# Performance work log

Measured on AMD Instinct MI355X. Metric: run time of the kernel, lower is better.

The kernel has to match this reference:

```python
import jax, jax.numpy as jnp
import numpy as np

DIM = 256
NHEAD = 8
HDIM = DIM // NHEAD
WS = 8
EPS = 1e-6
LN_EPS = 1e-5


def _layer_norm(x, g, b):
    m = x.mean(-1, keepdims=True)
    v = ((x - m) ** 2).mean(-1, keepdims=True)
    return (x - m) / jnp.sqrt(v + LN_EPS) * g + b


def _encoder_layer(x, Wq, Wk, Wv, Wm, Wmlp1, Wmlp2, g1, b1, g2, b2):
    # x: [n, L, C] windows; LoFTR encoder layer with linear (elu+1) attention
    n, L, C = x.shape
    q = (x @ Wq).reshape(n, L, NHEAD, HDIM)
    k = (x @ Wk).reshape(n, L, NHEAD, HDIM)
    v = (x @ Wv).reshape(n, L, NHEAD, HDIM)
    Q = jax.nn.elu(q) + 1.0
    K = jax.nn.elu(k) + 1.0
    v = v / L
    KV = jnp.einsum('nshd,nshv->nhdv', K, v)           # [n,H,D,D]
    Z = 1.0 / (jnp.einsum('nlhd,nhd->nlh', Q, K.sum(axis=1)) + EPS)
    msg = jnp.einsum('nlhd,nhdv,nlh->nlhv', Q, KV, Z) * L  # [n,L,H,D]
    msg = msg.reshape(n, L, C) @ Wm
    msg = _layer_norm(msg, g1, b1)
    h = jnp.concatenate([x, msg], axis=-1) @ Wmlp1     # [n,L,2C]
    h = jax.nn.relu(h) @ Wmlp2                          # [n,L,C]
    msg = _layer_norm(h, g2, b2)
    return msg + x


def setup_inputs() -> dict:
    key = jax.random.key(0)
    ks = jax.random.split(key, 12)
    B, Hh, Ww, C = 4, 240, 240, DIM
    x = jax.random.normal(ks[0], (B, Hh * Ww, C), dtype=jnp.float32)
    s = 0.02
    return {
        'x': x,
        'Wq': jax.random.normal(ks[1], (C, C), dtype=jnp.float32) * s,
        'Wk': jax.random.normal(ks[2], (C, C), dtype=jnp.float32) * s,
        'Wv': jax.random.normal(ks[3], (C, C), dtype=jnp.float32) * s,
        'Wm': jax.random.normal(ks[4], (C, C), dtype=jnp.float32) * s,
        'Wmlp1': jax.random.normal(ks[5], (2 * C, 2 * C), dtype=jnp.float32) * s,
        'Wmlp2': jax.random.normal(ks[6], (2 * C, C), dtype=jnp.float32) * s,
        'g1': jnp.ones((C,), dtype=jnp.float32),
        'b1': jnp.zeros((C,), dtype=jnp.float32),
        'g2': jnp.ones((C,), dtype=jnp.float32),
        'b2': jnp.zeros((C,), dtype=jnp.float32),
        'H': 240,
        'W': 240,
        'y': 0,
    }


def reference(x, Wq, Wk, Wv, Wm, Wmlp1, Wmlp2, g1, b1, g2, b2, H, W, y):
    B, N, C = x.shape
    # H, W chosen divisible by WS -> pad_r = pad_b = 0 (no-pad branch)
    _h, _w = H // WS, W // WS
    xw = x.reshape(B, _h, WS, _w, WS, C)
    xw = xw.transpose(0, 1, 3, 2, 4, 5).reshape(B * _h * _w, WS * WS, C)
    out = _encoder_layer(xw, Wq, Wk, Wv, Wm, Wmlp1, Wmlp2, g1, b1, g2, b2)
    out = out.reshape(B, _h, _w, WS, WS, C)
    out = out.transpose(0, 1, 3, 2, 4, 5).reshape(B, N, C)
    return out
```

## Files before the change

kernel.cpp:

```cpp
#include <hip/hip_runtime.h>

typedef unsigned short u16;
typedef unsigned int   u32;
typedef __attribute__((ext_vector_type(8))) short bf16x8;
typedef __attribute__((ext_vector_type(4))) float f32x4;

#define ATT_EPS 1e-6f
#define LN_EPS  1e-5f
#define MFMA16  __builtin_amdgcn_mfma_f32_16x16x32_bf16

__device__ __forceinline__ float bflo(u32 u){ return __uint_as_float(u << 16); }
__device__ __forceinline__ float bfhi(u32 u){ return __uint_as_float(u & 0xffff0000u); }
__device__ __forceinline__ u16 f2b(float f){
  u32 x = __float_as_uint(f);
  return (u16)((x + 0x7fffu + ((x >> 16) & 1u)) >> 16);
}
__device__ __forceinline__ float elup1(float x){ return x > 0.f ? x + 1.f : __expf(x); }
__device__ __forceinline__ bf16x8 as_bf(uint4 u){ union { uint4 a; bf16x8 b; } c; c.a = u; return c.b; }
__device__ __forceinline__ uint2 pack4(float a, float b, float c, float d){
  return make_uint2((u32)f2b(a) | ((u32)f2b(b) << 16),
                    (u32)f2b(c) | ((u32)f2b(d) << 16));
}

__device__ __forceinline__ int AO(int l, int cb){ return l*512 + (cb ^ ((l & 7) << 4)); }
__device__ __forceinline__ int TO(int c, int sb){ return c*128 + (sb ^ ((c & 7) << 4)); }
__device__ __forceinline__ int KVO(int h, int v, int db){ return h*4096 + v*64 + (db ^ ((v & 3) << 4)); }

__device__ __forceinline__ void qtr(float v[4], int qi){
  float x0 = __shfl_xor(v[0],1), x1 = __shfl_xor(v[1],1),
        x2 = __shfl_xor(v[2],1), x3 = __shfl_xor(v[3],1);
  if (qi & 1){ v[0]=x1; v[2]=x3; } else { v[1]=x0; v[3]=x2; }
  float y0 = __shfl_xor(v[0],2), y1 = __shfl_xor(v[1],2),
        y2 = __shfl_xor(v[2],2), y3 = __shfl_xor(v[3],2);
  if (qi & 2){ v[0]=y2; v[1]=y3; } else { v[2]=y0; v[3]=y1; }
}

__global__ __launch_bounds__(256)
void packw(const float* __restrict__ Wk, const float* __restrict__ Wv,
           const float* __restrict__ Wq, const float* __restrict__ Wm,
           const float* __restrict__ W1, const float* __restrict__ W2,
           uint4* __restrict__ ws)
{
  const int g = blockIdx.x*256 + threadIdx.x;
  const int tile = g >> 6, lane = g & 63;
  const float* src; int Nd, base, tl;
  if      (tile <  128){ src=Wk; Nd=256; base=0;     tl=tile;      }
  else if (tile <  256){ src=Wv; Nd=256; base=8192;  tl=tile-128;  }
  else if (tile <  384){ src=Wq; Nd=256; base=16384; tl=tile-256;  }
  else if (tile <  512){ src=Wm; Nd=256; base=24576; tl=tile-384;  }
  else if (tile < 1024){ src=W1; Nd=512; base=32768; tl=tile-512;  }
  else                 { src=W2; Nd=256; base=65536; tl=tile-1024; }
  const int KS = (tile >= 512) ? 16 : 8;
  const int nt = tl / KS, ks = tl - nt*KS;
  const int k0 = ks*32 + (lane >> 4)*8;
  const int n  = nt*16 + (lane & 15);
  u32 w[4];
  #pragma unroll
  for (int p = 0; p < 4; ++p){
    const u32 lo = f2b(src[(k0 + 2*p    )*Nd + n]);
    const u32 hi = f2b(src[(k0 + 2*p + 1)*Nd + n]);
    w[p] = lo | (hi << 16);
  }
  ws[base + (nt*KS + ks)*64 + lane] = make_uint4(w[0], w[1], w[2], w[3]);
}

__global__ __launch_bounds__(256, 2)
void lgattn_mfma(const float* __restrict__ xg, const uint4* __restrict__ wpk,
                 const float* __restrict__ g1v, const float* __restrict__ b1v,
                 const float* __restrict__ g2v, const float* __restrict__ b2v,
                 float* __restrict__ outg)
{
  __shared__ __align__(16) char  lds0[32768];
  __shared__ __align__(16) char  lds1[32768];
  __shared__ __align__(16) float ksum[256];
  __shared__ __align__(16) float denb[512];
  __shared__ __align__(16) float ps[256];

  const int t    = threadIdx.x;
  const int lane = t & 63;
  const int wid  = t >> 6;
  const int wm   = wid >> 1, wn = wid & 1;
  const int l15  = lane & 15, g4 = lane >> 4;
  const int qi   = lane & 3,  qq = (lane >> 2) & 3;
  const int rowA = 32*wm;
  const int wbn  = 8*wn;

  const int win = blockIdx.x;
  const int b   = win / 900;
  const int rem = win - b*900;
  const int wh  = rem / 30;
  const int ww  = rem - wh*30;
  const long long rowbase = ((long long)b*240 + wh*8)*240 + ww*8;

  const f32x4 fz = {0.f, 0.f, 0.f, 0.f};

  {
    const int r0 = wid*16, c0 = lane*4;
    #pragma unroll
    for (int i = 0; i < 16; ++i){
      const int l = r0 + i;
      const long long row = rowbase + (l >> 3)*240 + (l & 7);
      const float4 u = *(const float4*)(xg + row*256 + c0);
      *(uint2*)(lds0 + AO(l, c0*2)) = pack4(u.x, u.y, u.z, u.w);
    }
  }
  __syncthreads();

  bf16x8 xf[2][8];
  #pragma unroll
  for (int mt = 0; mt < 2; ++mt)
    #pragma unroll
    for (int ks = 0; ks < 8; ++ks)
      xf[mt][ks] = as_bf(*(const uint4*)(lds0 + AO(rowA + mt*16 + l15, ks*64 + g4*16)));
  __syncthreads();

  {
    f32x4 acc[8][2];
    #pragma unroll
    for (int nt = 0; nt < 8; ++nt){ acc[nt][0] = fz; acc[nt][1] = fz; }
    #pragma unroll
    for (int ks = 0; ks < 8; ++ks)
      #pragma unroll
      for (int nt = 0; nt < 8; ++nt){
        const bf16x8 bv = as_bf(wpk[((wbn + nt)*8 + ks)*64 + lane]);
        acc[nt][0] = MFMA16(xf[0][ks], bv, acc[nt][0], 0, 0, 0);
        acc[nt][1] = MFMA16(xf[1][ks], bv, acc[nt][1], 0, 0, 0);
      }
    #pragma unroll
    for (int nt = 0; nt < 8; ++nt)
      #pragma unroll
      for (int mt = 0; mt < 2; ++mt){
        const int c  = 128*wn + nt*16 + l15;
        const int sb = (rowA + mt*16 + 4*g4)*2;
        *(uint2*)(lds1 + TO(c, sb)) =
          pack4(elup1(acc[nt][mt][0]), elup1(acc[nt][mt][1]),
                elup1(acc[nt][mt][2]), elup1(acc[nt][mt][3]));
      }
  }
  {
    f32x4 acc[8][2];
    #pragma unroll
    for (int nt = 0; nt < 8; ++nt){ acc[nt][0] = fz; acc[nt][1] = fz; }
    #pragma unroll
    for (int ks = 0; ks < 8; ++ks)
      #pragma unroll
      for (int nt = 0; nt < 8; ++nt){
        const bf16x8 bv = as_bf(wpk[8192 + ((wbn + nt)*8 + ks)*64 + lane]);
        acc[nt][0] = MFMA16(xf[0][ks], bv, acc[nt][0], 0, 0, 0);
        acc[nt][1] = MFMA16(xf[1][ks], bv, acc[nt][1], 0, 0, 0);
      }
    #pragma unroll
    for (int nt = 0; nt < 8; ++nt)
      #pragma unroll
      for (int mt = 0; mt < 2; ++mt){
        const int c  = 128*wn + nt*16 + l15;
        const int sb = (rowA + mt*16 + 4*g4)*2;
        *(uint2*)(lds0 + TO(c, sb)) =
          pack4(acc[nt][mt][0], acc[nt][mt][1], acc[nt][mt][2], acc[nt][mt][3]);
      }
  }
  __syncthreads();

  {
    float s = 0.f;
    #pragma unroll
    for (int j = 0; j < 8; ++j){
      const uint4 u = *(const uint4*)(lds1 + TO(t, j*16));
      s += bflo(u.x)+bfhi(u.x)+bflo(u.y)+bfhi(u.y)
         + bflo(u.z)+bfhi(u.z)+bflo(u.w)+bfhi(u.w);
    }
    ksum[t] = s;
  }
  __syncthreads();

  {
    #pragma unroll
    for (int hh = 0; hh < 2; ++hh){
      const int h = 2*wid + hh;
      f32x4 acc[2][2];
      acc[0][0]=fz; acc[0][1]=fz; acc[1][0]=fz; acc[1][1]=fz;
      #pragma unroll
      for (int ks = 0; ks < 2; ++ks){
        bf16x8 a[2], bb[2];
        #pragma unroll
        for (int mt = 0; mt < 2; ++mt)
          a[mt]  = as_bf(*(const uint4*)(lds1 + TO(h*32 + mt*16 + l15, ks*64 + g4*16)));
        #pragma unroll
        for (int nt = 0; nt < 2; ++nt)
          bb[nt] = as_bf(*(const uint4*)(lds0 + TO(h*32 + nt*16 + l15, ks*64 + g4*16)));
        #pragma unroll
        for (int mt = 0; mt < 2; ++mt)
          #pragma unroll
          for (int nt = 0; nt < 2; ++nt)
            acc[mt][nt] = MFMA16(a[mt], bb[nt], acc[mt][nt], 0, 0, 0);
      }
      #pragma unroll
      for (int mt = 0; mt < 2; ++mt)
        #pragma unroll
        for (int nt = 0; nt < 2; ++nt){
          const int v  = nt*16 + l15;
          const int db = (mt*16 + 4*g4)*2;
          *(uint2*)(lds1 + KVO(h, v, db)) =
            pack4(acc[mt][nt][0], acc[mt][nt][1], acc[mt][nt][2], acc[mt][nt][3]);
        }
    }
  }
  __syncthreads();

  {
    f32x4 acc[8][2];
    #pragma unroll
    for (int nt = 0; nt < 8; ++nt){ acc[nt][0] = fz; acc[nt][1] = fz; }
    #pragma unroll
    for (int ks = 0; ks < 8; ++ks)
      #pragma unroll
      for (int nt = 0; nt < 8; ++nt){
        const bf16x8 bv = as_bf(wpk[16384 + ((wbn + nt)*8 + ks)*64 + lane]);
        acc[nt][0] = MFMA16(xf[0][ks], bv, acc[nt][0], 0, 0, 0);
        acc[nt][1] = MFMA16(xf[1][ks], bv, acc[nt][1], 0, 0, 0);
      }
    #pragma unroll
    for (int nt = 0; nt < 8; ++nt)
      #pragma unroll
      for (int mt = 0; mt < 2; ++mt){
        float v[4];
        #pragma unroll
        for (int r = 0; r < 4; ++r) v[r] = elup1(acc[nt][mt][r]);
        qtr(v, qi);
        const int l  = rowA + mt*16 + 4*g4 + qi;
        const int cb = (128*wn + nt*16 + 4*qq)*2;
        *(uint2*)(lds0 + AO(l, cb)) = pack4(v[0], v[1], v[2], v[3]);
      }
  }

  {
    const int dl = rowA + (lane & 31);
    #pragma unroll
    for (int hh = 0; hh < 2; ++hh){
      const int h = 4*wn + 2*(lane >> 5) + hh;
      float s = ATT_EPS;
      #pragma unroll
      for (int j = 0; j < 4; ++j){
        const uint4  qv = *(const uint4*)(lds0 + AO(dl, h*64 + j*16));
        const float4 k0 = *(const float4*)&ksum[h*32 + j*8];
        const float4 k1 = *(const float4*)&ksum[h*32 + j*8 + 4];
        s += bflo(qv.x)*k0.x + bfhi(qv.x)*k0.y + bflo(qv.y)*k0.z + bfhi(qv.y)*k0.w
           + bflo(qv.z)*k1.x + bfhi(qv.z)*k1.y + bflo(qv.w)*k1.z + bfhi(qv.w)*k1.w;
      }
      denb[dl*8 + h] = s;
    }
  }

  {
    f32x4 nacc[4][2][2];
    #pragma unroll
    for (int hh = 0; hh < 4; ++hh)
      #pragma unroll
      for (int mt = 0; mt < 2; ++mt)
        #pragma unroll
        for (int nt = 0; nt < 2; ++nt) nacc[hh][mt][nt] = fz;
    #pragma unroll
    for (int hh = 0; hh < 4; ++hh){
      const int h = 4*wn + hh;
      bf16x8 a[2], bb[2];
      #pragma unroll
      for (int mt = 0; mt < 2; ++mt)
        a[mt]  = as_bf(*(const uint4*)(lds0 + AO(rowA + mt*16 + l15, h*64 + g4*16)));
      #pragma unroll
      for (int nt = 0; nt < 2; ++nt)
        bb[nt] = as_bf(*(const uint4*)(lds1 + KVO(h, nt*16 + l15, g4*16)));
      #pragma unroll
      for (int mt = 0; mt < 2; ++mt)
        #pragma unroll
        for (int nt = 0; nt < 2; ++nt)
          nacc[hh][mt][nt] = MFMA16(a[mt], bb[nt], nacc[hh][mt][nt], 0, 0, 0);
    }
    __syncthreads();
    #pragma unroll
    for (int hh = 0; hh < 4; ++hh){
      const int h = 4*wn + hh;
      #pragma unroll
      for (int mt = 0; mt < 2; ++mt){
        const int   l  = rowA + mt*16 + 4*g4 + qi;
        const float rd = 1.0f / denb[l*8 + h];
        #pragma unroll
        for (int nt = 0; nt < 2; ++nt){
          float v[4];
          #pragma unroll
          for (int r = 0; r < 4; ++r) v[r] = nacc[hh][mt][nt][r];
          qtr(v, qi);
          const int cb = (h*32 + nt*16 + 4*qq)*2;
          *(uint2*)(lds1 + AO(l, cb)) = pack4(v[0]*rd, v[1]*rd, v[2]*rd, v[3]*rd);
        }
      }
    }
  }
  __syncthreads();

  {
    f32x4 macc[8][2];
    #pragma unroll
    for (int nt = 0; nt < 8; ++nt){ macc[nt][0] = fz; macc[nt][1] = fz; }
    #pragma unroll 2
    for (int ks = 0; ks < 8; ++ks){
      const bf16x8 a0 = as_bf(*(const uint4*)(lds1 + AO(rowA      + l15, ks*64 + g4*16)));
      const bf16x8 a1 = as_bf(*(const uint4*)(lds1 + AO(rowA + 16 + l15, ks*64 + g4*16)));
      #pragma unroll
      for (int nt = 0; nt < 8; ++nt){
        const bf16x8 bv = as_bf(wpk[24576 + ((wbn + nt)*8 + ks)*64 + lane]);
        macc[nt][0] = MFMA16(a0, bv, macc[nt][0], 0, 0, 0);
        macc[nt][1] = MFMA16(a1, bv, macc[nt][1], 0, 0, 0);
      }
    }
    float sm[2][4], sv[2][4];
    #pragma unroll
    for (int mt = 0; mt < 2; ++mt)
      #pragma unroll
      for (int r = 0; r < 4; ++r){
        float s = 0.f, q = 0.f;
        #pragma unroll
        for (int nt = 0; nt < 8; ++nt){ const float x = macc[nt][mt][r]; s += x; q += x*x; }
        #pragma unroll
        for (int m = 1; m < 16; m <<= 1){ s += __shfl_xor(s, m); q += __shfl_xor(q, m); }
        sm[mt][r] = s; sv[mt][r] = q;
      }
    if (l15 == 0){
      #pragma unroll
      for (int mt = 0; mt < 2; ++mt)
        #pragma unroll
        for (int r = 0; r < 4; ++r){
          const int row = rowA + mt*16 + 4*g4 + r;
          *(float2*)&ps[(row*2 + wn)*2] = make_float2(sm[mt][r], sv[mt][r]);
        }
    }
    __syncthreads();
    float mean[2][4], rstd[2][4];
    #pragma unroll
    for (int mt = 0; mt < 2; ++mt)
      #pragma unroll
      for (int r = 0; r < 4; ++r){
        const int row = rowA + mt*16 + 4*g4 + r;
        const float2 p0 = *(const float2*)&ps[(row*2 + 0)*2];
        const float2 p1 = *(const float2*)&ps[(row*2 + 1)*2];
        const float st = p0.x + p1.x, qt = p0.y + p1.y;
        const float mn = st * (1.f/256.f);
        mean[mt][r] = mn;
        rstd[mt][r] = rsqrtf(qt*(1.f/256.f) - mn*mn + LN_EPS);
      }
    #pragma unroll
    for (int mt = 0; mt < 2; ++mt){
      const int l = rowA + mt*16 + 4*g4 + qi;
      #pragma unroll
      for (int nt = 0; nt < 8; ++nt){
        float v[4];
        #pragma unroll
        for (int r = 0; r < 4; ++r) v[r] = (macc[nt][mt][r] - mean[mt][r]) * rstd[mt][r];
        qtr(v, qi);
        const int c = 128*wn + nt*16 + 4*qq;
        const float4 gg = *(const float4*)(g1v + c);
        const float4 bb = *(const float4*)(b1v + c);
        *(uint2*)(lds1 + AO(l, c*2)) =
          pack4(v[0]*gg.x + bb.x, v[1]*gg.y + bb.y, v[2]*gg.z + bb.z, v[3]*gg.w + bb.w);
      }
    }
  }
  __syncthreads();

  f32x4 oacc[8][2];
  #pragma unroll
  for (int nt = 0; nt < 8; ++nt){ oacc[nt][0] = fz; oacc[nt][1] = fz; }

  #pragma unroll
  for (int jt = 0; jt < 2; ++jt){
    f32x4 hacc[8][2];
    #pragma unroll
    for (int nt = 0; nt < 8; ++nt){ hacc[nt][0] = fz; hacc[nt][1] = fz; }
    const int w1base = 32768 + (jt*16 + wbn)*16*64;
    #pragma unroll
    for (int ks = 0; ks < 8; ++ks)
      #pragma unroll
      for (int nt = 0; nt < 8; ++nt){
        const bf16x8 bv = as_bf(wpk[w1base + (nt*16 + ks)*64 + lane]);
        hacc[nt][0] = MFMA16(xf[0][ks], bv, hacc[nt][0], 0, 0, 0);
        hacc[nt][1] = MFMA16(xf[1][ks], bv, hacc[nt][1], 0, 0, 0);
      }
    #pragma unroll 2
    for (int ks = 0; ks < 8; ++ks){
      const bf16x8 a0 = as_bf(*(const uint4*)(lds1 + AO(rowA      + l15, ks*64 + g4*16)));
      const bf16x8 a1 = as_bf(*(const uint4*)(lds1 + AO(rowA + 16 + l15, ks*64 + g4*16)));
      #pragma unroll
      for (int nt = 0; nt < 8; ++nt){
        const bf16x8 bv = as_bf(wpk[w1base + (nt*16 + 8 + ks)*64 + lane]);
        hacc[nt][0] = MFMA16(a0, bv, hacc[nt][0], 0, 0, 0);
        hacc[nt][1] = MFMA16(a1, bv, hacc[nt][1], 0, 0, 0);
      }
    }
    #pragma unroll
    for (int mt = 0; mt < 2; ++mt){
      const int l = rowA + mt*16 + 4*g4 + qi;
      #pragma unroll
      for (int nt = 0; nt < 8; ++nt){
        float v[4];
        #pragma unroll
        for (int r = 0; r < 4; ++r) v[r] = fmaxf(hacc[nt][mt][r], 0.f);
        qtr(v, qi);
        const int cb = (128*wn + nt*16 + 4*qq)*2;
        *(uint2*)(lds0 + AO(l, cb)) = pack4(v[0], v[1], v[2], v[3]);
      }
    }
    __syncthreads();
    #pragma unroll 2
    for (int ks = 0; ks < 8; ++ks){
      const bf16x8 a0 = as_bf(*(const uint4*)(lds0 + AO(rowA      + l15, ks*64 + g4*16)));
      const bf16x8 a1 = as_bf(*(const uint4*)(lds0 + AO(rowA + 16 + l15, ks*64 + g4*16)));
      #pragma unroll
      for (int nt = 0; nt < 8; ++nt){
        const bf16x8 bv = as_bf(wpk[65536 + ((wbn + nt)*16 + jt*8 + ks)*64 + lane]);
        oacc[nt][0] = MFMA16(a0, bv, oacc[nt][0], 0, 0, 0);
        oacc[nt][1] = MFMA16(a1, bv, oacc[nt][1], 0, 0, 0);
      }
    }
    if (jt == 0) __syncthreads();
  }

  {
    float sm[2][4], sv[2][4];
    #pragma unroll
    for (int mt = 0; mt < 2; ++mt)
      #pragma unroll
      for (int r = 0; r < 4; ++r){
        float s = 0.f, q = 0.f;
        #pragma unroll
        for (int nt = 0; nt < 8; ++nt){ const float x = oacc[nt][mt][r]; s += x; q += x*x; }
        #pragma unroll
        for (int m = 1; m < 16; m <<= 1){ s += __shfl_xor(s, m); q += __shfl_xor(q, m); }
        sm[mt][r] = s; sv[mt][r] = q;
      }
    __syncthreads();
    if (l15 == 0){
      #pragma unroll
      for (int mt = 0; mt < 2; ++mt)
        #pragma unroll
        for (int r = 0; r < 4; ++r){
          const int row = rowA + mt*16 + 4*g4 + r;
          *(float2*)&ps[(row*2 + wn)*2] = make_float2(sm[mt][r], sv[mt][r]);
        }
    }
    __syncthreads();
    float mean[2][4], rstd[2][4];
    #pragma unroll
    for (int mt = 0; mt < 2; ++mt)
      #pragma unroll
      for (int r = 0; r < 4; ++r){
        const int row = rowA + mt*16 + 4*g4 + r;
        const float2 p0 = *(const float2*)&ps[(row*2 + 0)*2];
        const float2 p1 = *(const float2*)&ps[(row*2 + 1)*2];
        const float st = p0.x + p1.x, qt = p0.y + p1.y;
        const float mn = st * (1.f/256.f);
        mean[mt][r] = mn;
        rstd[mt][r] = rsqrtf(qt*(1.f/256.f) - mn*mn + LN_EPS);
      }
    #pragma unroll
    for (int mt = 0; mt < 2; ++mt){
      const int l = rowA + mt*16 + 4*g4 + qi;
      const long long row = rowbase + (l >> 3)*240 + (l & 7);
      #pragma unroll
      for (int nt = 0; nt < 8; ++nt){
        float v[4];
        #pragma unroll
        for (int r = 0; r < 4; ++r) v[r] = (oacc[nt][mt][r] - mean[mt][r]) * rstd[mt][r];
        qtr(v, qi);
        const int c = 128*wn + nt*16 + 4*qq;
        const float4 gg = *(const float4*)(g2v + c);
        const float4 bb = *(const float4*)(b2v + c);
        const float4 xu = *(const float4*)(xg + row*256 + c);
        float4 st;
        st.x = v[0]*gg.x + bb.x + xu.x;
        st.y = v[1]*gg.y + bb.y + xu.y;
        st.z = v[2]*gg.z + bb.z + xu.z;
        st.w = v[3]*gg.w + bb.w + xu.w;
        *(float4*)(outg + row*256 + c) = st;
      }
    }
  }
}

extern "C" void kernel_launch(void* const* d_in, const int* in_sizes, int n_in,
                              void* d_out, int out_size, void* d_ws, size_t ws_size,
                              hipStream_t stream) {
  const float* xg = (const float*)d_in[0];
  const float* Wq = (const float*)d_in[1];
  const float* Wk = (const float*)d_in[2];
  const float* Wv = (const float*)d_in[3];
  const float* Wm = (const float*)d_in[4];
  const float* W1 = (const float*)d_in[5];
  const float* W2 = (const float*)d_in[6];
  const float* g1 = (const float*)d_in[7];
  const float* b1 = (const float*)d_in[8];
  const float* g2 = (const float*)d_in[9];
  const float* b2 = (const float*)d_in[10];

  uint4* wpk = (uint4*)d_ws;
  packw<<<dim3(320), dim3(256), 0, stream>>>(Wk, Wv, Wq, Wm, W1, W2, wpk);

  const int B = in_sizes[0] / (240 * 240 * 256);
  lgattn_mfma<<<dim3(B * 900), dim3(256), 0, stream>>>(xg, wpk, g1, b1, g2, b2, (float*)d_out);
}
```

Before: 1.488 ms.

## Use 8 waves per window block and fuse K-sum into KV computation

Doubles the block to 512 threads (8 waves in a 2x4 grid), so each wave computes half as many output column tiles in every GEMM stage, and the layer-norm partial sums are reduced across 4 column waves. The K column sum is now computed inside the per-head KV MFMA pass from the same loaded fragments, which removes one barrier and a separate LDS pass. The intent is more waves in flight to hide latency and fewer accumulator registers per wave, at the cost of more weight-fragment reloads per block and a tighter register budget under launch_bounds(512,4). Some loops are also fully unrolled.

```diff
diff --git a/kernel.cpp b/kernel.cpp
--- a/kernel.cpp
+++ b/kernel.cpp
@@ -64,7 +64,7 @@
   ws[base + (nt*KS + ks)*64 + lane] = make_uint4(w[0], w[1], w[2], w[3]);
 }
 
-__global__ __launch_bounds__(256, 2)
+__global__ __launch_bounds__(512, 4)
 void lgattn_mfma(const float* __restrict__ xg, const uint4* __restrict__ wpk,
                  const float* __restrict__ g1v, const float* __restrict__ b1v,
                  const float* __restrict__ g2v, const float* __restrict__ b2v,
@@ -74,16 +74,16 @@
   __shared__ __align__(16) char  lds1[32768];
   __shared__ __align__(16) float ksum[256];
   __shared__ __align__(16) float denb[512];
-  __shared__ __align__(16) float ps[256];
+  __shared__ __align__(16) float ps[512];
 
   const int t    = threadIdx.x;
   const int lane = t & 63;
   const int wid  = t >> 6;
-  const int wm   = wid >> 1, wn = wid & 1;
+  const int wm   = wid >> 2, wn = wid & 3;
   const int l15  = lane & 15, g4 = lane >> 4;
   const int qi   = lane & 3,  qq = (lane >> 2) & 3;
   const int rowA = 32*wm;
-  const int wbn  = 8*wn;
+  const int wbn  = 4*wn;
 
   const int win = blockIdx.x;
   const int b   = win / 900;
@@ -95,9 +95,9 @@
   const f32x4 fz = {0.f, 0.f, 0.f, 0.f};
 
   {
-    const int r0 = wid*16, c0 = lane*4;
-    #pragma unroll
-    for (int i = 0; i < 16; ++i){
+    const int r0 = wid*8, c0 = lane*4;
+    #pragma unroll
+    for (int i = 0; i < 8; ++i){
       const int l = r0 + i;
       const long long row = rowbase + (l >> 3)*240 + (l & 7);
       const float4 u = *(const float4*)(xg + row*256 + c0);
@@ -115,22 +115,22 @@
   __syncthreads();
 
   {
-    f32x4 acc[8][2];
-    #pragma unroll
-    for (int nt = 0; nt < 8; ++nt){ acc[nt][0] = fz; acc[nt][1] = fz; }
+    f32x4 acc[4][2];
+    #pragma unroll
+    for (int nt = 0; nt < 4; ++nt){ acc[nt][0] = fz; acc[nt][1] = fz; }
     #pragma unroll
     for (int ks = 0; ks < 8; ++ks)
       #pragma unroll
-      for (int nt = 0; nt < 8; ++nt){
+      for (int nt = 0; nt < 4; ++nt){
         const bf16x8 bv = as_bf(wpk[((wbn + nt)*8 + ks)*64 + lane]);
         acc[nt][0] = MFMA16(xf[0][ks], bv, acc[nt][0], 0, 0, 0);
         acc[nt][1] = MFMA16(xf[1][ks], bv, acc[nt][1], 0, 0, 0);
       }
     #pragma unroll
-    for (int nt = 0; nt < 8; ++nt)
+    for (int nt = 0; nt < 4; ++nt)
       #pragma unroll
       for (int mt = 0; mt < 2; ++mt){
-        const int c  = 128*wn + nt*16 + l15;
+        const int c  = 64*wn + nt*16 + l15;
         const int sb = (rowA + mt*16 + 4*g4)*2;
         *(uint2*)(lds1 + TO(c, sb)) =
           pack4(elup1(acc[nt][mt][0]), elup1(acc[nt][mt][1]),
@@ -138,22 +138,22 @@
       }
   }
   {
-    f32x4 acc[8][2];
-    #pragma unroll
-    for (int nt = 0; nt < 8; ++nt){ acc[nt][0] = fz; acc[nt][1] = fz; }
+    f32x4 acc[4][2];
+    #pragma unroll
+    for (int nt = 0; nt < 4; ++nt){ acc[nt][0] = fz; acc[nt][1] = fz; }
     #pragma unroll
     for (int ks = 0; ks < 8; ++ks)
       #pragma unroll
-      for (int nt = 0; nt < 8; ++nt){
+      for (int nt = 0; nt < 4; ++nt){
         const bf16x8 bv = as_bf(wpk[8192 + ((wbn + nt)*8 + ks)*64 + lane]);
         acc[nt][0] = MFMA16(xf[0][ks], bv, acc[nt][0], 0, 0, 0);
         acc[nt][1] = MFMA16(xf[1][ks], bv, acc[nt][1], 0, 0, 0);
       }
     #pragma unroll
-    for (int nt = 0; nt < 8; ++nt)
+    for (int nt = 0; nt < 4; ++nt)
       #pragma unroll
       for (int mt = 0; mt < 2; ++mt){
-        const int c  = 128*wn + nt*16 + l15;
+        const int c  = 64*wn + nt*16 + l15;
         const int sb = (rowA + mt*16 + 4*g4)*2;
         *(uint2*)(lds0 + TO(c, sb)) =
           pack4(acc[nt][mt][0], acc[nt][mt][1], acc[nt][mt][2], acc[nt][mt][3]);
@@ -162,65 +162,65 @@
   __syncthreads();
 
   {
-    float s = 0.f;
-    #pragma unroll
-    for (int j = 0; j < 8; ++j){
-      const uint4 u = *(const uint4*)(lds1 + TO(t, j*16));
-      s += bflo(u.x)+bfhi(u.x)+bflo(u.y)+bfhi(u.y)
-         + bflo(u.z)+bfhi(u.z)+bflo(u.w)+bfhi(u.w);
-    }
-    ksum[t] = s;
+    const int h = wid;
+    f32x4 acc[2][2];
+    acc[0][0]=fz; acc[0][1]=fz; acc[1][0]=fz; acc[1][1]=fz;
+    uint4 araw[2][2];
+    #pragma unroll
+    for (int ks = 0; ks < 2; ++ks)
+      #pragma unroll
+      for (int mt = 0; mt < 2; ++mt)
+        araw[ks][mt] = *(const uint4*)(lds1 + TO(h*32 + mt*16 + l15, ks*64 + g4*16));
+    #pragma unroll
+    for (int ks = 0; ks < 2; ++ks){
+      bf16x8 bb[2];
+      #pragma unroll
+      for (int nt = 0; nt < 2; ++nt)
+        bb[nt] = as_bf(*(const uint4*)(lds0 + TO(h*32 + nt*16 + l15, ks*64 + g4*16)));
+      #pragma unroll
+      for (int mt = 0; mt < 2; ++mt)
+        #pragma unroll
+        for (int nt = 0; nt < 2; ++nt)
+          acc[mt][nt] = MFMA16(as_bf(araw[ks][mt]), bb[nt], acc[mt][nt], 0, 0, 0);
+    }
+    float sm0 = 0.f, sm1 = 0.f;
+    #pragma unroll
+    for (int ks = 0; ks < 2; ++ks){
+      const uint4 u0 = araw[ks][0], u1 = araw[ks][1];
+      sm0 += bflo(u0.x)+bfhi(u0.x)+bflo(u0.y)+bfhi(u0.y)
+           + bflo(u0.z)+bfhi(u0.z)+bflo(u0.w)+bfhi(u0.w);
+      sm1 += bflo(u1.x)+bfhi(u1.x)+bflo(u1.y)+bfhi(u1.y)
+           + bflo(u1.z)+bfhi(u1.z)+bflo(u1.w)+bfhi(u1.w);
+    }
+    sm0 += __shfl_xor(sm0, 16); sm0 += __shfl_xor(sm0, 32);
+    sm1 += __shfl_xor(sm1, 16); sm1 += __shfl_xor(sm1, 32);
+    if (lane < 16){ ksum[h*32 + l15] = sm0; ksum[h*32 + 16 + l15] = sm1; }
+    #pragma unroll
+    for (int mt = 0; mt < 2; ++mt)
+      #pragma unroll
+      for (int nt = 0; nt < 2; ++nt){
+        const int v  = nt*16 + l15;
+        const int db = (mt*16 + 4*g4)*2;
+        *(uint2*)(lds1 + KVO(h, v, db)) =
+          pack4(acc[mt][nt][0], acc[mt][nt][1], acc[mt][nt][2], acc[mt][nt][3]);
+      }
   }
   __syncthreads();
 
   {
-    #pragma unroll
-    for (int hh = 0; hh < 2; ++hh){
-      const int h = 2*wid + hh;
-      f32x4 acc[2][2];
-      acc[0][0]=fz; acc[0][1]=fz; acc[1][0]=fz; acc[1][1]=fz;
-      #pragma unroll
-      for (int ks = 0; ks < 2; ++ks){
-        bf16x8 a[2], bb[2];
-        #pragma unroll
-        for (int mt = 0; mt < 2; ++mt)
-          a[mt]  = as_bf(*(const uint4*)(lds1 + TO(h*32 + mt*16 + l15, ks*64 + g4*16)));
-        #pragma unroll
-        for (int nt = 0; nt < 2; ++nt)
-          bb[nt] = as_bf(*(const uint4*)(lds0 + TO(h*32 + nt*16 + l15, ks*64 + g4*16)));
-        #pragma unroll
-        for (int mt = 0; mt < 2; ++mt)
-          #pragma unroll
-          for (int nt = 0; nt < 2; ++nt)
-            acc[mt][nt] = MFMA16(a[mt], bb[nt], acc[mt][nt], 0, 0, 0);
-      }
-      #pragma unroll
-      for (int mt = 0; mt < 2; ++mt)
-        #pragma unroll
-        for (int nt = 0; nt < 2; ++nt){
-          const int v  = nt*16 + l15;
-          const int db = (mt*16 + 4*g4)*2;
-          *(uint2*)(lds1 + KVO(h, v, db)) =
-            pack4(acc[mt][nt][0], acc[mt][nt][1], acc[mt][nt][2], acc[mt][nt][3]);
-        }
-    }
-  }
-  __syncthreads();
-
-  {
-    f32x4 acc[8][2];
-    #pragma unroll
-    for (int nt = 0; nt < 8; ++nt){ acc[nt][0] = fz; acc[nt][1] = fz; }
+    f32x4 acc[4][2];
+    #pragma unroll
+    for (int nt = 0; nt < 4; ++nt){ acc[nt][0] = fz; acc[nt][1] = fz; }
     #pragma unroll
     for (int ks = 0; ks < 8; ++ks)
       #pragma unroll
-      for (int nt = 0; nt < 8; ++nt){
+      for (int nt = 0; nt < 4; ++nt){
         const bf16x8 bv = as_bf(wpk[16384 + ((wbn + nt)*8 + ks)*64 + lane]);
         acc[nt][0] = MFMA16(xf[0][ks], bv, acc[nt][0], 0, 0, 0);
         acc[nt][1] = MFMA16(xf[1][ks], bv, acc[nt][1], 0, 0, 0);
       }
     #pragma unroll
-    for (int nt = 0; nt < 8; ++nt)
+    for (int nt = 0; nt < 4; ++nt)
       #pragma unroll
       for (int mt = 0; mt < 2; ++mt){
         float v[4];
@@ -228,40 +228,37 @@
         for (int r = 0; r < 4; ++r) v[r] = elup1(acc[nt][mt][r]);
         qtr(v, qi);
         const int l  = rowA + mt*16 + 4*g4 + qi;
-        const int cb = (128*wn + nt*16 + 4*qq)*2;
+        const int cb = (64*wn + nt*16 + 4*qq)*2;
         *(uint2*)(lds0 + AO(l, cb)) = pack4(v[0], v[1], v[2], v[3]);
       }
   }
 
   {
     const int dl = rowA + (lane & 31);
+    const int h  = 2*wn + (lane >> 5);
+    float s = ATT_EPS;
+    #pragma unroll
+    for (int j = 0; j < 4; ++j){
+      const uint4  qv = *(const uint4*)(lds0 + AO(dl, h*64 + j*16));
+      const float4 k0 = *(const float4*)&ksum[h*32 + j*8];
+      const float4 k1 = *(const float4*)&ksum[h*32 + j*8 + 4];
+      s += bflo(qv.x)*k0.x + bfhi(qv.x)*k0.y + bflo(qv.y)*k0.z + bfhi(qv.y)*k0.w
+         + bflo(qv.z)*k1.x + bfhi(qv.z)*k1.y + bflo(qv.w)*k1.z + bfhi(qv.w)*k1.w;
+    }
+    denb[dl*8 + h] = s;
+  }
+
+  {
+    f32x4 nacc[2][2][2];
+    #pragma unroll
+    for (int hh = 0; hh < 2; ++hh)
+      #pragma unroll
+      for (int mt = 0; mt < 2; ++mt)
+        #pragma unroll
+        for (int nt = 0; nt < 2; ++nt) nacc[hh][mt][nt] = fz;
     #pragma unroll
     for (int hh = 0; hh < 2; ++hh){
-      const int h = 4*wn + 2*(lane >> 5) + hh;
-      float s = ATT_EPS;
-      #pragma unroll
-      for (int j = 0; j < 4; ++j){
-        const uint4  qv = *(const uint4*)(lds0 + AO(dl, h*64 + j*16));
-        const float4 k0 = *(const float4*)&ksum[h*32 + j*8];
-        const float4 k1 = *(const float4*)&ksum[h*32 + j*8 + 4];
-        s += bflo(qv.x)*k0.x + bfhi(qv.x)*k0.y + bflo(qv.y)*k0.z + bfhi(qv.y)*k0.w
-           + bflo(qv.z)*k1.x + bfhi(qv.z)*k1.y + bflo(qv.w)*k1.z + bfhi(qv.w)*k1.w;
-      }
-      denb[dl*8 + h] = s;
-    }
-  }
-
-  {
-    f32x4 nacc[4][2][2];
-    #pragma unroll
-    for (int hh = 0; hh < 4; ++hh)
-      #pragma unroll
-      for (int mt = 0; mt < 2; ++mt)
-        #pragma unroll
-        for (int nt = 0; nt < 2; ++nt) nacc[hh][mt][nt] = fz;
-    #pragma unroll
-    for (int hh = 0; hh < 4; ++hh){
-      const int h = 4*wn + hh;
+      const int h = 2*wn + hh;
       bf16x8 a[2], bb[2];
       #pragma unroll
       for (int mt = 0; mt < 2; ++mt)
@@ -277,8 +274,8 @@
     }
     __syncthreads();
     #pragma unroll
-    for (int hh = 0; hh < 4; ++hh){
-      const int h = 4*wn + hh;
+    for (int hh = 0; hh < 2; ++hh){
+      const int h = 2*wn + hh;
       #pragma unroll
       for (int mt = 0; mt < 2; ++mt){
         const int   l  = rowA + mt*16 + 4*g4 + qi;
@@ -298,15 +295,15 @@
   __syncthreads();
 
   {
-    f32x4 macc[8][2];
-    #pragma unroll
-    for (int nt = 0; nt < 8; ++nt){ macc[nt][0] = fz; macc[nt][1] = fz; }
-    #pragma unroll 2
+    f32x4 macc[4][2];
+    #pragma unroll
+    for (int nt = 0; nt < 4; ++nt){ macc[nt][0] = fz; macc[nt][1] = fz; }
+    #pragma unroll
     for (int ks = 0; ks < 8; ++ks){
       const bf16x8 a0 = as_bf(*(const uint4*)(lds1 + AO(rowA      + l15, ks*64 + g4*16)));
       const bf16x8 a1 = as_bf(*(const uint4*)(lds1 + AO(rowA + 16 + l15, ks*64 + g4*16)));
       #pragma unroll
-      for (int nt = 0; nt < 8; ++nt){
+      for (int nt = 0; nt < 4; ++nt){
         const bf16x8 bv = as_bf(wpk[24576 + ((wbn + nt)*8 + ks)*64 + lane]);
         macc[nt][0] = MFMA16(a0, bv, macc[nt][0], 0, 0, 0);
         macc[nt][1] = MFMA16(a1, bv, macc[nt][1], 0, 0, 0);
@@ -319,7 +316,7 @@
       for (int r = 0; r < 4; ++r){
         float s = 0.f, q = 0.f;
         #pragma unroll
-        for (int nt = 0; nt < 8; ++nt){ const float x = macc[nt][mt][r]; s += x; q += x*x; }
+        for (int nt = 0; nt < 4; ++nt){ const float x = macc[nt][mt][r]; s += x; q += x*x; }
         #pragma unroll
         for (int m = 1; m < 16; m <<= 1){ s += __shfl_xor(s, m); q += __shfl_xor(q, m); }
         sm[mt][r] = s; sv[mt][r] = q;
@@ -330,7 +327,7 @@
         #pragma unroll
         for (int r = 0; r < 4; ++r){
           const int row = rowA + mt*16 + 4*g4 + r;
-          *(float2*)&ps[(row*2 + wn)*2] = make_float2(sm[mt][r], sv[mt][r]);
+          *(float2*)&ps[(row*4 + wn)*2] = make_float2(sm[mt][r], sv[mt][r]);
         }
     }
     __syncthreads();
@@ -340,9 +337,12 @@
       #pragma unroll
       for (int r = 0; r < 4; ++r){
         const int row = rowA + mt*16 + 4*g4 + r;
-        const float2 p0 = *(const float2*)&ps[(row*2 + 0)*2];
-        const float2 p1 = *(const float2*)&ps[(row*2 + 1)*2];
-        const float st = p0.x + p1.x, qt = p0.y + p1.y;
+        float st = 0.f, qt = 0.f;
+        #pragma unroll
+        for (int w = 0; w < 4; ++w){
+          const float2 p = *(const float2*)&ps[(row*4 + w)*2];
+          st += p.x; qt += p.y;
+        }
         const float mn = st * (1.f/256.f);
         mean[mt][r] = mn;
         rstd[mt][r] = rsqrtf(qt*(1.f/256.f) - mn*mn + LN_EPS);
@@ -351,12 +351,12 @@
     for (int mt = 0; mt < 2; ++mt){
       const int l = rowA + mt*16 + 4*g4 + qi;
       #pragma unroll
-      for (int nt = 0; nt < 8; ++nt){
+      for (int nt = 0; nt < 4; ++nt){
         float v[4];
         #pragma unroll
         for (int r = 0; r < 4; ++r) v[r] = (macc[nt][mt][r] - mean[mt][r]) * rstd[mt][r];
         qtr(v, qi);
-        const int c = 128*wn + nt*16 + 4*qq;
+        const int c = 64*wn + nt*16 + 4*qq;
         const float4 gg = *(const float4*)(g1v + c);
         const float4 bb = *(const float4*)(b1v + c);
         *(uint2*)(lds1 + AO(l, c*2)) =
@@ -366,31 +366,30 @@
   }
   __syncthreads();
 
-  f32x4 oacc[8][2];
+  f32x4 oacc[4][2];
   #pragma unroll
-  for (int nt = 0; nt < 8; ++nt){ oacc[nt][0] = fz; oacc[nt][1] = fz; }
+  for (int nt = 0; nt < 4; ++nt){ oacc[nt][0] = fz; oacc[nt][1] = fz; }
 
   #pragma unroll
   for (int jt = 0; jt < 2; ++jt){
-    f32x4 hacc[8][2];
-    #pragma unroll
-    for (int nt = 0; nt < 8; ++nt){ hacc[nt][0] = fz; hacc[nt][1] = fz; }
-    const int w1base = 32768 + (jt*16 + wbn)*16*64;
+    f32x4 hacc[4][2];
+    #pragma unroll
+    for (int nt = 0; nt < 4; ++nt){ hacc[nt][0] = fz; hacc[nt][1] = fz; }
     #pragma unroll
     for (int ks = 0; ks < 8; ++ks)
       #pragma unroll
-      for (int nt = 0; nt < 8; ++nt){
-        const bf16x8 bv = as_bf(wpk[w1base + (nt*16 + ks)*64 + lane]);
+      for (int nt = 0; nt < 4; ++nt){
+        const bf16x8 bv = as_bf(wpk[32768 + ((jt*16 + wbn + nt)*16 + ks)*64 + lane]);
         hacc[nt][0] = MFMA16(xf[0][ks], bv, hacc[nt][0], 0, 0, 0);
         hacc[nt][1] = MFMA16(xf[1][ks], bv, hacc[nt][1], 0, 0, 0);
       }
-    #pragma unroll 2
+    #pragma unroll
     for (int ks = 0; ks < 8; ++ks){
       const bf16x8 a0 = as_bf(*(const uint4*)(lds1 + AO(rowA      + l15, ks*64 + g4*16)));
       const bf16x8 a1 = as_bf(*(const uint4*)(lds1 + AO(rowA + 16 + l15, ks*64 + g4*16)));
       #pragma unroll
-      for (int nt = 0; nt < 8; ++nt){
-        const bf16x8 bv = as_bf(wpk[w1base + (nt*16 + 8 + ks)*64 + lane]);
+      for (int nt = 0; nt < 4; ++nt){
+        const bf16x8 bv = as_bf(wpk[32768 + ((jt*16 + wbn + nt)*16 + 8 + ks)*64 + lane]);
         hacc[nt][0] = MFMA16(a0, bv, hacc[nt][0], 0, 0, 0);
         hacc[nt][1] = MFMA16(a1, bv, hacc[nt][1], 0, 0, 0);
       }
@@ -399,22 +398,22 @@
     for (int mt = 0; mt < 2; ++mt){
       const int l = rowA + mt*16 + 4*g4 + qi;
       #pragma unroll
-      for (int nt = 0; nt < 8; ++nt){
+      for (int nt = 0; nt < 4; ++nt){
         float v[4];
         #pragma unroll
         for (int r = 0; r < 4; ++r) v[r] = fmaxf(hacc[nt][mt][r], 0.f);
         qtr(v, qi);
-        const int cb = (128*wn + nt*16 + 4*qq)*2;
+        const int cb = (64*wn + nt*16 + 4*qq)*2;
         *(uint2*)(lds0 + AO(l, cb)) = pack4(v[0], v[1], v[2], v[3]);
       }
     }
     __syncthreads();
-    #pragma unroll 2
+    #pragma unroll
     for (int ks = 0; ks < 8; ++ks){
       const bf16x8 a0 = as_bf(*(const uint4*)(lds0 + AO(rowA      + l15, ks*64 + g4*16)));
       const bf16x8 a1 = as_bf(*(const uint4*)(lds0 + AO(rowA + 16 + l15, ks*64 + g4*16)));
       #pragma unroll
-      for (int nt = 0; nt < 8; ++nt){
+      for (int nt = 0; nt < 4; ++nt){
         const bf16x8 bv = as_bf(wpk[65536 + ((wbn + nt)*16 + jt*8 + ks)*64 + lane]);
         oacc[nt][0] = MFMA16(a0, bv, oacc[nt][0], 0, 0, 0);
         oacc[nt][1] = MFMA16(a1, bv, oacc[nt][1], 0, 0, 0);
@@ -431,19 +430,18 @@
       for (int r = 0; r < 4; ++r){
         float s = 0.f, q = 0.f;
         #pragma unroll
-        for (int nt = 0; nt < 8; ++nt){ const float x = oacc[nt][mt][r]; s += x; q += x*x; }
+        for (int nt = 0; nt < 4; ++nt){ const float x = oacc[nt][mt][r]; s += x; q += x*x; }
         #pragma unroll
         for (int m = 1; m < 16; m <<= 1){ s += __shfl_xor(s, m); q += __shfl_xor(q, m); }
         sm[mt][r] = s; sv[mt][r] = q;
       }
-    __syncthreads();
     if (l15 == 0){
       #pragma unroll
       for (int mt = 0; mt < 2; ++mt)
         #pragma unroll
         for (int r = 0; r < 4; ++r){
           const int row = rowA + mt*16 + 4*g4 + r;
-          *(float2*)&ps[(row*2 + wn)*2] = make_float2(sm[mt][r], sv[mt][r]);
+          *(float2*)&ps[(row*4 + wn)*2] = make_float2(sm[mt][r], sv[mt][r]);
         }
     }
     __syncthreads();
@@ -453,9 +451,12 @@
       #pragma unroll
       for (int r = 0; r < 4; ++r){
         const int row = rowA + mt*16 + 4*g4 + r;
-        const float2 p0 = *(const float2*)&ps[(row*2 + 0)*2];
-        const float2 p1 = *(const float2*)&ps[(row*2 + 1)*2];
-        const float st = p0.x + p1.x, qt = p0.y + p1.y;
+        float st = 0.f, qt = 0.f;
+        #pragma unroll
+        for (int w = 0; w < 4; ++w){
+          const float2 p = *(const float2*)&ps[(row*4 + w)*2];
+          st += p.x; qt += p.y;
+        }
         const float mn = st * (1.f/256.f);
         mean[mt][r] = mn;
         rstd[mt][r] = rsqrtf(qt*(1.f/256.f) - mn*mn + LN_EPS);
@@ -465,12 +466,12 @@
       const int l = rowA + mt*16 + 4*g4 + qi;
       const long long row = rowbase + (l >> 3)*240 + (l & 7);
       #pragma unroll
-      for (int nt = 0; nt < 8; ++nt){
+      for (int nt = 0; nt < 4; ++nt){
         float v[4];
         #pragma unroll
         for (int r = 0; r < 4; ++r) v[r] = (oacc[nt][mt][r] - mean[mt][r]) * rstd[mt][r];
         qtr(v, qi);
-        const int c = 128*wn + nt*16 + 4*qq;
+        const int c = 64*wn + nt*16 + 4*qq;
         const float4 gg = *(const float4*)(g2v + c);
         const float4 bb = *(const float4*)(b2v + c);
         const float4 xu = *(const float4*)(xg + row*256 + c);
@@ -504,5 +505,5 @@
   packw<<<dim3(320), dim3(256), 0, stream>>>(Wk, Wv, Wq, Wm, W1, W2, wpk);
 
   const int B = in_sizes[0] / (240 * 240 * 256);
-  lgattn_mfma<<<dim3(B * 900), dim3(256), 0, stream>>>(xg, wpk, g1, b1, g2, b2, (float*)d_out);
+  lgattn_mfma<<<dim3(B * 900), dim3(512), 0, stream>>>(xg, wpk, g1, b1, g2, b2, (float*)d_out);
 }
```

New measurement: 1.610 ms. +8.2%, slower.
